# Performance work log

Hardware: AMD Instinct MI355X
Metric: run time of the kernel (lower is better)

Reference implementation:

```python
import jax, jax.numpy as jnp
import numpy as np

B, T, D, F, H, HID, OUT = 256, 512, 768, 1024, 8, 512, 256
EPS = 1e-5

def setup_inputs() -> dict:
    key = jax.random.key(0)
    ks = jax.random.split(key, 16)
    s = lambda fan_in: 1.0 / np.sqrt(fan_in)
    return {
        "x": jax.random.normal(ks[0], (B, F), jnp.float32),
        "text_feat": jax.random.normal(ks[1], (B, T, D), jnp.float32),
        "attention_mask": jax.random.randint(ks[2], (B, T), 0, 2, jnp.int32),
        # cross-attention params (torch Linear weight layout [out,in])
        "Wq": jax.random.normal(ks[3], (F, F), jnp.float32) * s(F),
        "bq": jnp.zeros((F,), jnp.float32),
        "Wk": jax.random.normal(ks[4], (F, D), jnp.float32) * s(D),
        "bk": jnp.zeros((F,), jnp.float32),
        "Wv": jax.random.normal(ks[5], (F, D), jnp.float32) * s(D),
        "bv": jnp.zeros((F,), jnp.float32),
        "Wo": jax.random.normal(ks[6], (F, F), jnp.float32) * s(F),
        "bo": jnp.zeros((F,), jnp.float32),
        # MLP: hidden Linear -> BatchNorm1d -> GELU, then output Linear
        "W1": jax.random.normal(ks[7], (HID, F), jnp.float32) * s(F),
        "b1": jnp.zeros((HID,), jnp.float32),
        "gamma": jnp.ones((HID,), jnp.float32),
        "beta": jnp.zeros((HID,), jnp.float32),
        "W2": jax.random.normal(ks[8], (OUT, HID), jnp.float32) * s(HID),
        "b2": jnp.zeros((OUT,), jnp.float32),
    }

def _forward(x, text_feat, attention_mask, Wq, bq, Wk, bk, Wv, bv, Wo, bo,
             W1, b1, gamma, beta, W2, b2):
    d = F // H
    q = (x @ Wq.T + bq).reshape(B, H, d)                      # [B,H,d] (q_len=1)
    k = (text_feat @ Wk.T + bk).reshape(B, T, H, d)           # [B,T,H,d]
    v = (text_feat @ Wv.T + bv).reshape(B, T, H, d)
    attn = jnp.einsum('bhd,bthd->bht', q, k) / jnp.sqrt(jnp.float32(d))
    attn = jnp.where(attention_mask[:, None, :] == 0, -jnp.inf, attn)
    attn = jax.nn.softmax(attn, axis=-1)                       # [B,H,T]
    out = jnp.einsum('bht,bthd->bhd', attn, v).reshape(B, F)
    out = out @ Wo.T + bo
    # MLP hidden: linear -> BatchNorm1d (training batch stats) -> GELU (exact)
    h = out @ W1.T + b1
    mu = jnp.mean(h, axis=0)
    var = jnp.var(h, axis=0)
    h = (h - mu) / jnp.sqrt(var + EPS) * gamma + beta
    h = jax.nn.gelu(h, approximate=False)
    return h @ W2.T + b2

def reference(x, text_feat, attention_mask, Wq, bq, Wk, bk, Wv, bv, Wo, bo,
              W1, b1, gamma, beta, W2, b2):
    return _forward(x, text_feat, attention_mask, Wq, bq, Wk, bk, Wv, bv, Wo, bo,
                    W1, b1, gamma, beta, W2, b2)
```

## Files before the change

### kernel.cpp

```cpp
#include <hip/hip_runtime.h>
#include <math.h>

#define Bb   256
#define Tt   512
#define Dd   768
#define Ff   1024
#define Hh   8
#define HIDh 512
#define OUTo 256

__device__ __forceinline__ void tr_tile4(const float* __restrict__ in,
                                         float* __restrict__ out,
                                         int R, int C, int cx, int ry,
                                         float (*tile)[33])
{
    int c0 = cx * 32, r0 = ry * 32;
    int r  = threadIdx.x >> 3;
    int c4 = (threadIdx.x & 7) * 4;
    float4 v = *(const float4*)&in[(size_t)(r0 + r) * C + c0 + c4];
    tile[r][c4 + 0] = v.x;
    tile[r][c4 + 1] = v.y;
    tile[r][c4 + 2] = v.z;
    tile[r][c4 + 3] = v.w;
    __syncthreads();
    float4 o;
    o.x = tile[c4 + 0][r];
    o.y = tile[c4 + 1][r];
    o.z = tile[c4 + 2][r];
    o.w = tile[c4 + 3][r];
    *(float4*)&out[(size_t)(c0 + r) * R + r0 + c4] = o;
}

__global__ __launch_bounds__(256) void prep(const float* __restrict__ Wq, float* __restrict__ WqT,
                                            const float* __restrict__ Wo, float* __restrict__ WoT,
                                            const float* __restrict__ Wv, float* __restrict__ WvT,
                                            const float* __restrict__ W1, float* __restrict__ W1T,
                                            const float* __restrict__ W2, float* __restrict__ W2T,
                                            const float* __restrict__ Wk, float* __restrict__ WkT)
{
    __shared__ float tile[32][33];
    int idx = blockIdx.x;
    if (idx < 1024) {
        tr_tile4(Wq, WqT, 1024, 1024, idx & 31, idx >> 5, tile);
    } else if (idx < 2048) {
        int i2 = idx - 1024;
        tr_tile4(Wo, WoT, 1024, 1024, i2 & 31, i2 >> 5, tile);
    } else if (idx < 2816) {
        int i2 = idx - 2048;
        tr_tile4(Wv, WvT, 1024, 768, i2 % 24, i2 / 24, tile);
    } else if (idx < 3328) {
        int i2 = idx - 2816;
        tr_tile4(W1, W1T, 512, 1024, i2 & 31, i2 >> 5, tile);
    } else if (idx < 3456) {
        int i2 = idx - 3328;
        tr_tile4(W2, W2T, 256, 512, i2 & 15, i2 >> 4, tile);
    } else {
        int i2 = idx - 3456;
        int i = i2 >> 3, h = i2 & 7;
        if (threadIdx.x < 192) {
            int j = threadIdx.x * 4;
            *(float4*)&WkT[(size_t)(i * 8 + h) * 768 + j] =
                *(const float4*)&Wk[(size_t)(h * 128 + i) * 768 + j];
        }
    }
}

#define FMA16(acc, a, w0, w1, w2, w3)                         \
    acc.x = fmaf(a.x, w0.x, acc.x); acc.y = fmaf(a.x, w0.y, acc.y); \
    acc.z = fmaf(a.x, w0.z, acc.z); acc.w = fmaf(a.x, w0.w, acc.w); \
    acc.x = fmaf(a.y, w1.x, acc.x); acc.y = fmaf(a.y, w1.y, acc.y); \
    acc.z = fmaf(a.y, w1.z, acc.z); acc.w = fmaf(a.y, w1.w, acc.w); \
    acc.x = fmaf(a.z, w2.x, acc.x); acc.y = fmaf(a.z, w2.y, acc.y); \
    acc.z = fmaf(a.z, w2.z, acc.z); acc.w = fmaf(a.z, w2.w, acc.w); \
    acc.x = fmaf(a.w, w3.x, acc.x); acc.y = fmaf(a.w, w3.y, acc.y); \
    acc.z = fmaf(a.w, w3.z, acc.z); acc.w = fmaf(a.w, w3.w, acc.w);

template<int CT, int RT, int R, int KS>
__global__ __launch_bounds__(256, 4) void gemm_sk(const float* __restrict__ A, int strideA,
                                                  const float* __restrict__ Wt, int N,
                                                  float* __restrict__ Cslab, int M)
{
    constexpr int CG = CT / 4;
    constexpr int RG = RT / R;
    static_assert(CG * RG == 256, "bad tile");
    const int cg = threadIdx.x % CG;
    const int rg = threadIdx.x / CG;
    const int n0 = blockIdx.x * CT + cg * 4;
    const int r0 = blockIdx.y * RT;
    const int k0 = blockIdx.z * KS;

    __shared__ float As[RT][KS + 4];
    for (int e = threadIdx.x * 4; e < RT * KS; e += 1024) {
        int r = e / KS, k = e % KS;
        *(float4*)&As[r][k] = *(const float4*)&A[(size_t)(r0 + r) * strideA + k0 + k];
    }
    __syncthreads();

    float4 acc[R];
#pragma unroll
    for (int rr = 0; rr < R; ++rr) acc[rr] = make_float4(0.f, 0.f, 0.f, 0.f);
    const float* wp = Wt + (size_t)k0 * N + n0;
#pragma unroll 2
    for (int k = 0; k < KS; k += 4) {
        float4 w0 = *(const float4*)&wp[(size_t)(k + 0) * N];
        float4 w1 = *(const float4*)&wp[(size_t)(k + 1) * N];
        float4 w2 = *(const float4*)&wp[(size_t)(k + 2) * N];
        float4 w3 = *(const float4*)&wp[(size_t)(k + 3) * N];
#pragma unroll
        for (int rr = 0; rr < R; ++rr) {
            float4 a = *(const float4*)&As[rg * R + rr][k];
            FMA16(acc[rr], a, w0, w1, w2, w3)
        }
    }
    float* cp = Cslab + (size_t)blockIdx.z * M * N;
#pragma unroll
    for (int rr = 0; rr < R; ++rr)
        *(float4*)&cp[(size_t)(r0 + rg * R + rr) * N + n0] = acc[rr];
}

template<int S>
__global__ __launch_bounds__(256) void reduce_add(const float* __restrict__ slabs,
                                                  size_t slabstride,
                                                  const float* __restrict__ bias,
                                                  float* __restrict__ out, int N, int total)
{
    int i4 = (blockIdx.x * 256 + threadIdx.x) * 4;
    if (i4 >= total) return;
    float4 acc = *(const float4*)&bias[i4 % N];
#pragma unroll
    for (int s = 0; s < S; ++s) {
        float4 v = *(const float4*)(slabs + (size_t)s * slabstride + i4);
        acc.x += v.x; acc.y += v.y; acc.z += v.z; acc.w += v.w;
    }
    *(float4*)&out[i4] = acc;
}

__global__ __launch_bounds__(256, 4) void qk_gemm(const float* __restrict__ qfull,
                                                  const float* __restrict__ WkT,
                                                  float* __restrict__ qkfull)
{
    const int cg = threadIdx.x & 15;
    const int rg = threadIdx.x >> 4;
    const int cb = blockIdx.x, rb = blockIdx.y;
    const int n0 = cb * 64 + cg * 4;
    const int r0 = rb * 64;
    const int aoff = ((cb * 64) / 768) * 128;

    __shared__ float As[64][132];
    for (int e = threadIdx.x * 4; e < 64 * 128; e += 1024) {
        int r = e >> 7, k = e & 127;
        *(float4*)&As[r][k] = *(const float4*)&qfull[(size_t)(r0 + r) * 1024 + aoff + k];
    }
    __syncthreads();

    float4 acc[4];
#pragma unroll
    for (int rr = 0; rr < 4; ++rr) acc[rr] = make_float4(0.f, 0.f, 0.f, 0.f);
    const float* wp = WkT + n0;
#pragma unroll 2
    for (int k = 0; k < 128; k += 4) {
        float4 w0 = *(const float4*)&wp[(size_t)(k + 0) * 6144];
        float4 w1 = *(const float4*)&wp[(size_t)(k + 1) * 6144];
        float4 w2 = *(const float4*)&wp[(size_t)(k + 2) * 6144];
        float4 w3 = *(const float4*)&wp[(size_t)(k + 3) * 6144];
#pragma unroll
        for (int rr = 0; rr < 4; ++rr) {
            float4 a = *(const float4*)&As[rg * 4 + rr][k];
            FMA16(acc[rr], a, w0, w1, w2, w3)
        }
    }
#pragma unroll
    for (int rr = 0; rr < 4; ++rr)
        *(float4*)&qkfull[(size_t)(r0 + rg * 4 + rr) * 6144 + n0] = acc[rr];
}

__device__ __forceinline__ float dot12(float4 a0, float4 a1, float4 a2,
                                       float4 x0, float4 x1, float4 x2)
{
    float acc;
    acc = a0.x * x0.x;
    acc = fmaf(a0.y, x0.y, acc);
    acc = fmaf(a0.z, x0.z, acc);
    acc = fmaf(a0.w, x0.w, acc);
    acc = fmaf(a1.x, x1.x, acc);
    acc = fmaf(a1.y, x1.y, acc);
    acc = fmaf(a1.z, x1.z, acc);
    acc = fmaf(a1.w, x1.w, acc);
    acc = fmaf(a2.x, x2.x, acc);
    acc = fmaf(a2.y, x2.y, acc);
    acc = fmaf(a2.z, x2.z, acc);
    acc = fmaf(a2.w, x2.w, acc);
    return acc;
}

__global__ __launch_bounds__(256, 2) void attn_part(const float* __restrict__ text,
                                                    const int* __restrict__ mask,
                                                    const float* __restrict__ qk,
                                                    float* __restrict__ pctx,
                                                    float* __restrict__ psum)
{
    const int bx   = blockIdx.x;
    const int b    = bx >> 2;
    const int qt   = bx & 3;
    const int tid  = threadIdx.x;
    const int wv   = tid >> 6;
    const int lane = tid & 63;

    __shared__ float qk_s[Hh][Dd];
    __shared__ float ctx_s[Hh][Dd];
    __shared__ float wsum_s[4][Hh];
    __shared__ int   list_s[128];
    __shared__ int   wcnt_s[2];

    const float* qkp = qk + (size_t)b * (Hh * Dd);
    float* qf = (float*)qk_s;
    float* cf = (float*)ctx_s;
    for (int e = tid * 4; e < Hh * Dd; e += 1024) {
        *(float4*)&qf[e] = *(const float4*)&qkp[e];
        *(float4*)&cf[e] = make_float4(0.f, 0.f, 0.f, 0.f);
    }

    int m = 0, pre = 0, t = 0;
    if (wv < 2) {
        t = qt * 128 + wv * 64 + lane;
        m = mask[(size_t)b * Tt + t];
        unsigned long long bal = __ballot(m != 0);
        pre = __popcll(bal & ((1ull << lane) - 1ull));
        if (lane == 0) wcnt_s[wv] = __popcll(bal);
    }
    __syncthreads();
    if (wv < 2 && m) {
        int base = wv ? wcnt_s[0] : 0;
        list_s[base + pre] = t;
    }
    __syncthreads();
    const int cnt = wcnt_s[0] + wcnt_s[1];

    float s[Hh] = {0.f, 0.f, 0.f, 0.f, 0.f, 0.f, 0.f, 0.f};
    float4 cr[Hh][3];
#pragma unroll
    for (int h = 0; h < Hh; ++h)
#pragma unroll
        for (int c = 0; c < 3; ++c) cr[h][c] = make_float4(0.f, 0.f, 0.f, 0.f);

    const float scale = 0.08838834764831845f;
    const float* tbase = text + (size_t)b * Tt * Dd;

    int e = wv;
    float4 xa0, xa1, xa2, xb0, xb1, xb2;
    xa0 = xa1 = xa2 = make_float4(0.f, 0.f, 0.f, 0.f);
    xb0 = xb1 = xb2 = xa0;
    if (e < cnt) {
        const float* tp = tbase + (size_t)list_s[e] * Dd + 4 * lane;
        xa0 = *(const float4*)(tp);
        xa1 = *(const float4*)(tp + 256);
        xa2 = *(const float4*)(tp + 512);
        int e1 = (e + 4 < cnt) ? e + 4 : cnt - 1;
        const float* tq = tbase + (size_t)list_s[e1] * Dd + 4 * lane;
        xb0 = *(const float4*)(tq);
        xb1 = *(const float4*)(tq + 256);
        xb2 = *(const float4*)(tq + 512);
    }
    while (e < cnt) {
        int ei = (e + 8 < cnt) ? e + 8 : cnt - 1;
        const float* tc = tbase + (size_t)list_s[ei] * Dd + 4 * lane;
        float4 xc0 = *(const float4*)(tc);
        float4 xc1 = *(const float4*)(tc + 256);
        float4 xc2 = *(const float4*)(tc + 512);

        float p[Hh];
#pragma unroll
        for (int h = 0; h < Hh; ++h) {
            const float* qh = &qk_s[h][4 * lane];
            float4 a0 = *(const float4*)(qh);
            float4 a1 = *(const float4*)(qh + 256);
            float4 a2 = *(const float4*)(qh + 512);
            p[h] = dot12(a0, a1, a2, xa0, xa1, xa2);
        }
#pragma unroll
        for (int h = 0; h < Hh; ++h) {
            float v = p[h];
            v += __shfl_xor(v, 1);
            v += __shfl_xor(v, 2);
            v += __shfl_xor(v, 4);
            v += __shfl_xor(v, 8);
            v += __shfl_xor(v, 16);
            v += __shfl_xor(v, 32);
            float w = __expf(v * scale);
            s[h] += w;
            cr[h][0].x = fmaf(w, xa0.x, cr[h][0].x);
            cr[h][0].y = fmaf(w, xa0.y, cr[h][0].y);
            cr[h][0].z = fmaf(w, xa0.z, cr[h][0].z);
            cr[h][0].w = fmaf(w, xa0.w, cr[h][0].w);
            cr[h][1].x = fmaf(w, xa1.x, cr[h][1].x);
            cr[h][1].y = fmaf(w, xa1.y, cr[h][1].y);
            cr[h][1].z = fmaf(w, xa1.z, cr[h][1].z);
            cr[h][1].w = fmaf(w, xa1.w, cr[h][1].w);
            cr[h][2].x = fmaf(w, xa2.x, cr[h][2].x);
            cr[h][2].y = fmaf(w, xa2.y, cr[h][2].y);
            cr[h][2].z = fmaf(w, xa2.z, cr[h][2].z);
            cr[h][2].w = fmaf(w, xa2.w, cr[h][2].w);
        }
        xa0 = xb0; xa1 = xb1; xa2 = xb2;
        xb0 = xc0; xb1 = xc1; xb2 = xc2;
        e += 4;
    }

    if (lane == 0) {
#pragma unroll
        for (int h = 0; h < Hh; ++h) wsum_s[wv][h] = s[h];
    }

    for (int w4 = 0; w4 < 4; ++w4) {
        __syncthreads();
        if (wv == w4) {
#pragma unroll
            for (int h = 0; h < Hh; ++h) {
                float* cp = &ctx_s[h][4 * lane];
#pragma unroll
                for (int c = 0; c < 3; ++c) {
                    float4 cur = *(float4*)(cp + c * 256);
                    cur.x += cr[h][c].x;
                    cur.y += cr[h][c].y;
                    cur.z += cr[h][c].z;
                    cur.w += cr[h][c].w;
                    *(float4*)(cp + c * 256) = cur;
                }
            }
        }
    }
    __syncthreads();

    if (tid < Hh) {
        float S = wsum_s[0][tid] + wsum_s[1][tid] + wsum_s[2][tid] + wsum_s[3][tid];
        psum[(size_t)bx * Hh + tid] = S;
    }
    float* outp = pctx + (size_t)bx * (Hh * Dd);
    for (int e2 = tid * 4; e2 < Hh * Dd; e2 += 1024)
        *(float4*)&outp[e2] = *(const float4*)&cf[e2];
}

__global__ __launch_bounds__(256, 4) void v_gemm(const float* __restrict__ pctx,
                                                 const float* __restrict__ psum,
                                                 const float* __restrict__ WvT,
                                                 float* __restrict__ aoslab)
{
    const int cg = threadIdx.x & 31;
    const int rg = threadIdx.x >> 5;
    const int h = blockIdx.x, rb = blockIdx.y, ks = blockIdx.z;
    const int n0 = h * 128 + cg * 4;
    const int r0 = rb * 32;
    const int k0 = ks * 128;

    __shared__ float As[32][132];
    __shared__ float sv[32];

    if (threadIdx.x < 32) {
        int row = r0 + threadIdx.x;
        float S = 0.f;
#pragma unroll
        for (int i = 0; i < 4; ++i) S += psum[(size_t)(row * 4 + i) * Hh + h];
        sv[threadIdx.x] = 1.0f / S;
    }
    __syncthreads();
    for (int e = threadIdx.x * 4; e < 32 * 128; e += 1024) {
        int r = e >> 7, k = e & 127;
        size_t col = (size_t)h * 768 + k0 + k;
        float4 acc = make_float4(0.f, 0.f, 0.f, 0.f);
#pragma unroll
        for (int i = 0; i < 4; ++i) {
            float4 v = *(const float4*)&pctx[((size_t)(r0 + r) * 4 + i) * 6144 + col];
            acc.x += v.x; acc.y += v.y; acc.z += v.z; acc.w += v.w;
        }
        float svv = sv[r];
        acc.x *= svv; acc.y *= svv; acc.z *= svv; acc.w *= svv;
        *(float4*)&As[r][k] = acc;
    }
    __syncthreads();

    float4 acc[4];
#pragma unroll
    for (int rr = 0; rr < 4; ++rr) acc[rr] = make_float4(0.f, 0.f, 0.f, 0.f);
    const float* wp = WvT + (size_t)k0 * 1024 + n0;
#pragma unroll 2
    for (int k = 0; k < 128; k += 4) {
        float4 w0 = *(const float4*)&wp[(size_t)(k + 0) * 1024];
        float4 w1 = *(const float4*)&wp[(size_t)(k + 1) * 1024];
        float4 w2 = *(const float4*)&wp[(size_t)(k + 2) * 1024];
        float4 w3 = *(const float4*)&wp[(size_t)(k + 3) * 1024];
#pragma unroll
        for (int rr = 0; rr < 4; ++rr) {
            float4 a = *(const float4*)&As[rg * 4 + rr][k];
            FMA16(acc[rr], a, w0, w1, w2, w3)
        }
    }
    float* cp = aoslab + (size_t)ks * 262144;
#pragma unroll
    for (int rr = 0; rr < 4; ++rr)
        *(float4*)&cp[(size_t)(r0 + rg * 4 + rr) * 1024 + n0] = acc[rr];
}

__global__ __launch_bounds__(256) void bn_stats2(const float* __restrict__ h1full,
                                                 const float* __restrict__ gamma,
                                                 const float* __restrict__ beta,
                                                 float* __restrict__ scl,
                                                 float* __restrict__ shf)
{
    int c8 = threadIdx.x & 7, rg = threadIdx.x >> 3;
    int c = blockIdx.x * 8 + c8;
    float sum = 0.f, sq = 0.f;
    for (int r = rg; r < Bb; r += 32) {
        float v = h1full[(size_t)r * HIDh + c];
        sum += v;
        sq = fmaf(v, v, sq);
    }
    __shared__ float ss[32][8], sq_[32][8];
    ss[rg][c8] = sum; sq_[rg][c8] = sq;
    for (int off = 16; off > 0; off >>= 1) {
        __syncthreads();
        if (rg < off) { ss[rg][c8] += ss[rg + off][c8]; sq_[rg][c8] += sq_[rg + off][c8]; }
    }
    __syncthreads();
    if (rg == 0) {
        float mu  = ss[0][c8] * (1.0f / Bb);
        float var = sq_[0][c8] * (1.0f / Bb) - mu * mu;
        float g   = gamma[c] * rsqrtf(var + 1e-5f);
        scl[c] = g;
        shf[c] = fmaf(-mu, g, beta[c]);
    }
}

__global__ __launch_bounds__(256, 4) void gelu2(const float* __restrict__ h1full,
                                                const float* __restrict__ scl,
                                                const float* __restrict__ shf,
                                                const float* __restrict__ W2T,
                                                const float* __restrict__ b2,
                                                float* __restrict__ out)
{
    const int cg = threadIdx.x & 15;
    const int rg = threadIdx.x >> 4;
    const int n0 = blockIdx.x * 64 + cg * 4;
    const int r0 = blockIdx.y * 16;

    __shared__ float As[16][132];
    float4 acc = make_float4(0.f, 0.f, 0.f, 0.f);

    for (int k0 = 0; k0 < HIDh; k0 += 128) {
        __syncthreads();
        for (int e = threadIdx.x * 4; e < 2048; e += 1024) {
            int r = e >> 7, k = e & 127;
            float4 v  = *(const float4*)&h1full[(size_t)(r0 + r) * HIDh + k0 + k];
            float4 sc = *(const float4*)&scl[k0 + k];
            float4 sh = *(const float4*)&shf[k0 + k];
            float4 z;
            z.x = fmaf(v.x, sc.x, sh.x);
            z.y = fmaf(v.y, sc.y, sh.y);
            z.z = fmaf(v.z, sc.z, sh.z);
            z.w = fmaf(v.w, sc.w, sh.w);
            z.x = 0.5f * z.x * (1.0f + erff(z.x * 0.70710678118654752f));
            z.y = 0.5f * z.y * (1.0f + erff(z.y * 0.70710678118654752f));
            z.z = 0.5f * z.z * (1.0f + erff(z.z * 0.70710678118654752f));
            z.w = 0.5f * z.w * (1.0f + erff(z.w * 0.70710678118654752f));
            *(float4*)&As[r][k] = z;
        }
        __syncthreads();
        const float* wp = W2T + (size_t)k0 * OUTo + n0;
#pragma unroll 2
        for (int k = 0; k < 128; k += 4) {
            float4 w0 = *(const float4*)&wp[(size_t)(k + 0) * OUTo];
            float4 w1 = *(const float4*)&wp[(size_t)(k + 1) * OUTo];
            float4 w2 = *(const float4*)&wp[(size_t)(k + 2) * OUTo];
            float4 w3 = *(const float4*)&wp[(size_t)(k + 3) * OUTo];
            float4 a = *(const float4*)&As[rg][k];
            FMA16(acc, a, w0, w1, w2, w3)
        }
    }

    float4 bvv = *(const float4*)&b2[n0];
    acc.x += bvv.x; acc.y += bvv.y; acc.z += bvv.z; acc.w += bvv.w;
    *(float4*)&out[(size_t)(r0 + rg) * OUTo + n0] = acc;
}

extern "C" void kernel_launch(void* const* d_in, const int* in_sizes, int n_in,
                              void* d_out, int out_size, void* d_ws, size_t ws_size,
                              hipStream_t stream)
{
    const float* x     = (const float*)d_in[0];
    const float* text  = (const float*)d_in[1];
    const int*   amask = (const int*)d_in[2];
    const float* Wq    = (const float*)d_in[3];
    const float* bq    = (const float*)d_in[4];
    const float* Wk    = (const float*)d_in[5];
    const float* Wv    = (const float*)d_in[7];
    const float* bv    = (const float*)d_in[8];
    const float* Wo    = (const float*)d_in[9];
    const float* bo    = (const float*)d_in[10];
    const float* W1    = (const float*)d_in[11];
    const float* b1    = (const float*)d_in[12];
    const float* gamma = (const float*)d_in[13];
    const float* beta  = (const float*)d_in[14];
    const float* W2    = (const float*)d_in[15];
    const float* b2    = (const float*)d_in[16];

    float* ws     = (float*)d_ws;
    float* WqT    = ws;
    float* WoT    = WqT    + 1048576;
    float* WkT    = WoT    + 1048576;
    float* WvT    = WkT    + 786432;
    float* W1T    = WvT    + 786432;
    float* W2T    = W1T    + 524288;
    float* qslab  = W2T    + 131072;
    float* qfull  = qslab  + 2097152;
    float* qkfull = qfull  + 262144;
    float* pctx   = qkfull + 1572864;
    float* psum   = pctx   + 6291456;
    float* aoslab = psum   + 8192;
    float* aofull = aoslab + 1572864;
    float* oslab  = aofull + 262144;
    float* ofull  = oslab  + 2097152;
    float* h1slab = ofull  + 262144;
    float* h1full = h1slab + 1048576;
    float* scl    = h1full + 131072;
    float* shf    = scl    + 512;

    prep<<<4480, 256, 0, stream>>>(Wq, WqT, Wo, WoT, Wv, WvT, W1, W1T, W2, W2T, Wk, WkT);

    gemm_sk<64, 64, 4, 128><<<dim3(16, 4, 8), 256, 0, stream>>>(x, 1024, WqT, 1024, qslab, 256);
    reduce_add<8><<<256, 256, 0, stream>>>(qslab, 262144, bq, qfull, 1024, 262144);

    qk_gemm<<<dim3(96, 4), 256, 0, stream>>>(qfull, WkT, qkfull);

    attn_part<<<1024, 256, 0, stream>>>(text, amask, qkfull, pctx, psum);

    v_gemm<<<dim3(8, 8, 6), 256, 0, stream>>>(pctx, psum, WvT, aoslab);
    reduce_add<6><<<256, 256, 0, stream>>>(aoslab, 262144, bv, aofull, 1024, 262144);

    gemm_sk<64, 64, 4, 128><<<dim3(16, 4, 8), 256, 0, stream>>>(aofull, 1024, WoT, 1024, oslab, 256);
    reduce_add<8><<<256, 256, 0, stream>>>(oslab, 262144, bo, ofull, 1024, 262144);

    gemm_sk<64, 64, 4, 128><<<dim3(8, 4, 8), 256, 0, stream>>>(ofull, 1024, W1T, 512, h1slab, 256);
    reduce_add<8><<<128, 256, 0, stream>>>(h1slab, 131072, b1, h1full, 512, 131072);

    bn_stats2<<<64, 256, 0, stream>>>(h1full, gamma, beta, scl, shf);

    gelu2<<<dim3(4, 16), 256, 0, stream>>>(h1full, scl, shf, W2T, b2, (float*)d_out);
}
```

Before: 202.9 us.

## Deepen attention prefetch, unroll GEMM k-loops, fuse split-K reduce into BN stats

The attention kernel prefetches text rows three iterations ahead instead of two, to hide more global load latency at the cost of more registers. Several GEMM inner loops are unrolled by 4 instead of 2. The split-K reduction for the W1 GEMM is folded into the BatchNorm statistics kernel, removing one launch and one pass over h1. The fused kernel reads the slabs with scalar, column-strided loads across only 64 blocks, which may be slower than the separate vectorised reduce.

```diff
diff --git a/kernel.cpp b/kernel.cpp
--- a/kernel.cpp
+++ b/kernel.cpp
@@ -100,7 +100,7 @@
 #pragma unroll
     for (int rr = 0; rr < R; ++rr) acc[rr] = make_float4(0.f, 0.f, 0.f, 0.f);
     const float* wp = Wt + (size_t)k0 * N + n0;
-#pragma unroll 2
+#pragma unroll 4
     for (int k = 0; k < KS; k += 4) {
         float4 w0 = *(const float4*)&wp[(size_t)(k + 0) * N];
         float4 w1 = *(const float4*)&wp[(size_t)(k + 1) * N];
@@ -157,7 +157,7 @@
 #pragma unroll
     for (int rr = 0; rr < 4; ++rr) acc[rr] = make_float4(0.f, 0.f, 0.f, 0.f);
     const float* wp = WkT + n0;
-#pragma unroll 2
+#pragma unroll 4
     for (int k = 0; k < 128; k += 4) {
         float4 w0 = *(const float4*)&wp[(size_t)(k + 0) * 6144];
         float4 w1 = *(const float4*)&wp[(size_t)(k + 1) * 6144];
@@ -247,9 +247,10 @@
     const float* tbase = text + (size_t)b * Tt * Dd;
 
     int e = wv;
-    float4 xa0, xa1, xa2, xb0, xb1, xb2;
+    float4 xa0, xa1, xa2, xb0, xb1, xb2, xc0, xc1, xc2;
     xa0 = xa1 = xa2 = make_float4(0.f, 0.f, 0.f, 0.f);
     xb0 = xb1 = xb2 = xa0;
+    xc0 = xc1 = xc2 = xa0;
     if (e < cnt) {
         const float* tp = tbase + (size_t)list_s[e] * Dd + 4 * lane;
         xa0 = *(const float4*)(tp);
@@ -260,13 +261,18 @@
         xb0 = *(const float4*)(tq);
         xb1 = *(const float4*)(tq + 256);
         xb2 = *(const float4*)(tq + 512);
+        int e2 = (e + 8 < cnt) ? e + 8 : cnt - 1;
+        const float* tr = tbase + (size_t)list_s[e2] * Dd + 4 * lane;
+        xc0 = *(const float4*)(tr);
+        xc1 = *(const float4*)(tr + 256);
+        xc2 = *(const float4*)(tr + 512);
     }
     while (e < cnt) {
-        int ei = (e + 8 < cnt) ? e + 8 : cnt - 1;
-        const float* tc = tbase + (size_t)list_s[ei] * Dd + 4 * lane;
-        float4 xc0 = *(const float4*)(tc);
-        float4 xc1 = *(const float4*)(tc + 256);
-        float4 xc2 = *(const float4*)(tc + 512);
+        int ei = (e + 12 < cnt) ? e + 12 : cnt - 1;
+        const float* td = tbase + (size_t)list_s[ei] * Dd + 4 * lane;
+        float4 xd0 = *(const float4*)(td);
+        float4 xd1 = *(const float4*)(td + 256);
+        float4 xd2 = *(const float4*)(td + 512);
 
         float p[Hh];
 #pragma unroll
@@ -303,6 +309,7 @@
         }
         xa0 = xb0; xa1 = xb1; xa2 = xb2;
         xb0 = xc0; xb1 = xc1; xb2 = xc2;
+        xc0 = xd0; xc1 = xd1; xc2 = xd2;
         e += 4;
     }
 
@@ -382,7 +389,7 @@
 #pragma unroll
     for (int rr = 0; rr < 4; ++rr) acc[rr] = make_float4(0.f, 0.f, 0.f, 0.f);
     const float* wp = WvT + (size_t)k0 * 1024 + n0;
-#pragma unroll 2
+#pragma unroll 4
     for (int k = 0; k < 128; k += 4) {
         float4 w0 = *(const float4*)&wp[(size_t)(k + 0) * 1024];
         float4 w1 = *(const float4*)&wp[(size_t)(k + 1) * 1024];
@@ -400,17 +407,24 @@
         *(float4*)&cp[(size_t)(r0 + rg * 4 + rr) * 1024 + n0] = acc[rr];
 }
 
-__global__ __launch_bounds__(256) void bn_stats2(const float* __restrict__ h1full,
-                                                 const float* __restrict__ gamma,
-                                                 const float* __restrict__ beta,
-                                                 float* __restrict__ scl,
-                                                 float* __restrict__ shf)
+__global__ __launch_bounds__(256) void redbn(const float* __restrict__ h1slab,
+                                             const float* __restrict__ b1,
+                                             const float* __restrict__ gamma,
+                                             const float* __restrict__ beta,
+                                             float* __restrict__ h1full,
+                                             float* __restrict__ scl,
+                                             float* __restrict__ shf)
 {
     int c8 = threadIdx.x & 7, rg = threadIdx.x >> 3;
     int c = blockIdx.x * 8 + c8;
+    float bias = b1[c];
     float sum = 0.f, sq = 0.f;
     for (int r = rg; r < Bb; r += 32) {
-        float v = h1full[(size_t)r * HIDh + c];
+        float v = bias;
+#pragma unroll
+        for (int s = 0; s < 8; ++s)
+            v += h1slab[(size_t)s * 131072 + (size_t)r * HIDh + c];
+        h1full[(size_t)r * HIDh + c] = v;
         sum += v;
         sq = fmaf(v, v, sq);
     }
@@ -465,7 +479,7 @@
         }
         __syncthreads();
         const float* wp = W2T + (size_t)k0 * OUTo + n0;
-#pragma unroll 2
+#pragma unroll 4
         for (int k = 0; k < 128; k += 4) {
             float4 w0 = *(const float4*)&wp[(size_t)(k + 0) * OUTo];
             float4 w1 = *(const float4*)&wp[(size_t)(k + 1) * OUTo];
@@ -539,9 +553,8 @@
     reduce_add<8><<<256, 256, 0, stream>>>(oslab, 262144, bo, ofull, 1024, 262144);
 
     gemm_sk<64, 64, 4, 128><<<dim3(8, 4, 8), 256, 0, stream>>>(ofull, 1024, W1T, 512, h1slab, 256);
-    reduce_add<8><<<128, 256, 0, stream>>>(h1slab, 131072, b1, h1full, 512, 131072);
-
-    bn_stats2<<<64, 256, 0, stream>>>(h1full, gamma, beta, scl, shf);
+
+    redbn<<<64, 256, 0, stream>>>(h1slab, b1, gamma, beta, h1full, scl, shf);
 
     gelu2<<<dim3(4, 16), 256, 0, stream>>>(h1full, scl, shf, W2T, b2, (float*)d_out);
 }
```

Result: slower. 230.8 us (+13.7%).
